# Kernel optimization log

Hardware: AMD Instinct MI355X
Metric: run time of the kernel (lower is better)

The kernel has to match this reference:

```python
import jax, jax.numpy as jnp
import numpy as np
import math

GROUPS = 32
EPS = 1e-5
NUM_HEADS = 8


def group_norm(x, gamma, beta):
    # x: [B, C, H, W]; normalize within each of GROUPS channel groups over (C/G, H, W)
    B, C, H, W = x.shape
    xg = x.reshape(B, GROUPS, C // GROUPS, H, W)
    mean = jnp.mean(xg, axis=(2, 3, 4), keepdims=True)
    var = jnp.var(xg, axis=(2, 3, 4), keepdims=True)
    xn = ((xg - mean) * jax.lax.rsqrt(var + EPS)).reshape(B, C, H, W)
    return xn * gamma[None, :, None, None] + beta[None, :, None, None]


def setup_inputs() -> dict:
    key = jax.random.key(0)
    ks = jax.random.split(key, 10)
    C = 512
    B, H, W = 2, 64, 64
    s = 1.0 / math.sqrt(C)
    return {
        "x": jax.random.normal(ks[0], (B, C, H, W), jnp.float32),
        "gamma": jnp.ones((C,), jnp.float32),
        "beta": jnp.zeros((C,), jnp.float32),
        "Wq": jax.random.normal(ks[1], (C, C), jnp.float32) * s,
        "bq": jax.random.normal(ks[2], (C,), jnp.float32) * 0.01,
        "Wk": jax.random.normal(ks[3], (C, C), jnp.float32) * s,
        "bk": jax.random.normal(ks[4], (C,), jnp.float32) * 0.01,
        "Wv": jax.random.normal(ks[5], (C, C), jnp.float32) * s,
        "bv": jax.random.normal(ks[6], (C,), jnp.float32) * 0.01,
        "Wo": jax.random.normal(ks[7], (C, C), jnp.float32) * s,
        "bo": jax.random.normal(ks[8], (C,), jnp.float32) * 0.01,
    }


def reference(x, gamma, beta, Wq, bq, Wk, bk, Wv, bv, Wo, bo):
    B, C, H, W = x.shape
    N = H * W
    hd = C // NUM_HEADS
    h = group_norm(x, gamma, beta)
    h = h.reshape(B, C, N).transpose(0, 2, 1)  # [B, N, C]
    # torch nn.Linear: y = x @ W.T + b
    q = (h @ Wq.T + bq).reshape(B, N, NUM_HEADS, hd)
    k = (h @ Wk.T + bk).reshape(B, N, NUM_HEADS, hd)
    v = (h @ Wv.T + bv).reshape(B, N, NUM_HEADS, hd)
    scale = 1.0 / math.sqrt(hd)
    attn = jnp.einsum('bihd,bjhd->bijh', q, k) * scale  # [B, N, N, heads]
    attn = jax.nn.softmax(attn, axis=2)
    o = jnp.einsum('bijh,bjhd->bihd', attn, v).reshape(B, N, C)
    o = o @ Wo.T + bo
    o = o.transpose(0, 2, 1).reshape(B, C, H, W)
    return x + o
```

## Files before the change

### kernel.cpp

```cpp
#include <hip/hip_runtime.h>
#include <cstdint>
#include <cstddef>

typedef __bf16 bf16x8 __attribute__((ext_vector_type(8)));
typedef float f32x4 __attribute__((ext_vector_type(4)));
typedef float f32x16 __attribute__((ext_vector_type(16)));
typedef unsigned short ushort8 __attribute__((ext_vector_type(8)));
typedef unsigned u32x2 __attribute__((ext_vector_type(2)));
typedef float f4 __attribute__((ext_vector_type(4)));

__device__ __forceinline__ unsigned short f2bf(float f) {
    __bf16 b = (__bf16)f;
    return *(unsigned short*)&b;
}
__device__ __forceinline__ unsigned pk2bf(float a, float b) {
    __bf16 x = (__bf16)a, y = (__bf16)b;
    unsigned short ux = *(unsigned short*)&x, uy = *(unsigned short*)&y;
    return (unsigned)ux | ((unsigned)uy << 16);
}
__device__ __forceinline__ float bf2f(unsigned short u) {
    union { unsigned u; float f; } v; v.u = ((unsigned)u) << 16; return v.f;
}

#if __has_builtin(__builtin_amdgcn_exp2f)
#define EXP2(x) __builtin_amdgcn_exp2f(x)
#else
#define EXP2(x) exp2f(x)
#endif

__device__ __forceinline__ void pl32swap(unsigned& x, unsigned& y) {
#if __has_builtin(__builtin_amdgcn_permlane32_swap)
    auto r = __builtin_amdgcn_permlane32_swap(x, y, false, false);
    x = r[0]; y = r[1];
#else
    unsigned xs = (unsigned)__shfl_xor((int)x, 32, 64);
    unsigned ys = (unsigned)__shfl_xor((int)y, 32, 64);
    bool lo = ((threadIdx.x & 63) < 32);
    unsigned nx = lo ? x : ys;
    unsigned ny = lo ? xs : y;
    x = nx; y = ny;
#endif
}

#define GLL(g, l) __builtin_amdgcn_global_load_lds( \
    (__attribute__((address_space(1))) void*)(g), \
    (__attribute__((address_space(3))) void*)(l), 16, 0, 0)

#define CS 0.18033688011112042f

__global__ __launch_bounds__(256) void convert_w(
    const float* __restrict__ wq, const float* __restrict__ wk,
    const float* __restrict__ wv, const float* __restrict__ wo,
    unsigned short* __restrict__ out)
{
    int i = blockIdx.x * 256 + threadIdx.x;
    const float* src = (i < 262144) ? wq : (i < 524288) ? wk : (i < 786432) ? wv : wo;
    out[i] = f2bf(src[i & 262143]);
}

__global__ __launch_bounds__(256) void gn_stats(
    const float* __restrict__ x, float* __restrict__ part)
{
    const int q = blockIdx.x, bg = blockIdx.y;
    const f4* xv = (const f4*)(x + (size_t)bg * 65536 + q * 16384);
    float s = 0.f, sq = 0.f;
    for (int i = threadIdx.x; i < 4096; i += 256) {
        f4 v = xv[i];
        s  += v.x + v.y + v.z + v.w;
        sq += v.x * v.x + v.y * v.y + v.z * v.z + v.w * v.w;
    }
    #pragma unroll
    for (int off = 32; off > 0; off >>= 1) {
        s  += __shfl_xor(s, off, 64);
        sq += __shfl_xor(sq, off, 64);
    }
    __shared__ float red[8];
    const int w = threadIdx.x >> 6, lane = threadIdx.x & 63;
    if (lane == 0) { red[w] = s; red[4 + w] = sq; }
    __syncthreads();
    if (threadIdx.x == 0) {
        part[(bg * 4 + q) * 2]     = red[0] + red[1] + red[2] + red[3];
        part[(bg * 4 + q) * 2 + 1] = red[4] + red[5] + red[6] + red[7];
    }
}

__global__ __launch_bounds__(256) void gn_apply(
    const float* __restrict__ x, const float* __restrict__ gamma,
    const float* __restrict__ beta, const float* __restrict__ part,
    unsigned short* __restrict__ h)
{
    const int q = blockIdx.x, bg = blockIdx.y;
    const int b = bg >> 5, g = bg & 31;
    float s = 0.f, sq = 0.f;
    #pragma unroll
    for (int j = 0; j < 4; ++j) {
        s  += part[(bg * 4 + j) * 2];
        sq += part[(bg * 4 + j) * 2 + 1];
    }
    const float mean = s * (1.f / 65536.f);
    const float rstd = rsqrtf(sq * (1.f / 65536.f) - mean * mean + 1e-5f);

    float gm[16], bt[16];
    #pragma unroll
    for (int c = 0; c < 16; ++c) {
        gm[c] = gamma[g * 16 + c] * rstd;
        bt[c] = beta[g * 16 + c];
    }
    const float* xg = x + (size_t)bg * 65536;
    const int n0 = q * 1024 + threadIdx.x * 4;
    float val[16][4];
    #pragma unroll
    for (int c = 0; c < 16; ++c) {
        f4 v = *(const f4*)&xg[(size_t)c * 4096 + n0];
        val[c][0] = (v.x - mean) * gm[c] + bt[c];
        val[c][1] = (v.y - mean) * gm[c] + bt[c];
        val[c][2] = (v.z - mean) * gm[c] + bt[c];
        val[c][3] = (v.w - mean) * gm[c] + bt[c];
    }
    #pragma unroll
    for (int nn = 0; nn < 4; ++nn) {
        ushort8 v0, v1;
        #pragma unroll
        for (int c = 0; c < 8; ++c)  v0[c]     = f2bf(val[c][nn]);
        #pragma unroll
        for (int c = 8; c < 16; ++c) v1[c - 8] = f2bf(val[c][nn]);
        unsigned short* dst = h + ((size_t)(b * 4096 + n0 + nn)) * 512 + g * 16;
        *(ushort8*)dst = v0;
        *(ushort8*)(dst + 8) = v1;
    }
}

template <int MODE>
__global__ __launch_bounds__(256, 2) void gemm_bt(
    const unsigned short* __restrict__ A,
    const unsigned short* __restrict__ Bt,
    const float* __restrict__ bias0,
    const float* __restrict__ bias1,
    const float* __restrict__ bias2,
    const float* __restrict__ resid,
    void* __restrict__ outp,
    unsigned short* __restrict__ vtout,
    int M, int N, int K)
{
    __shared__ __attribute__((aligned(16))) unsigned short As[128 * 32];
    __shared__ __attribute__((aligned(16))) unsigned short Bs[128 * 32];
    const int t = threadIdx.x;
    const int w = t >> 6, lane = t & 63;
    const int l15 = lane & 15, l4 = lane >> 4;
    const int bm = blockIdx.y, bn = blockIdx.x;
    const int wm = (w >> 1) * 64, wn = (w & 1) * 64;

    f32x4 acc[4][4] = {};

    const int srow = t >> 2;
    const int sc8  = (t & 3) * 8;

    const unsigned short* gA0 = A  + (size_t)(bm * 128 + srow) * K + sc8;
    const unsigned short* gA1 = gA0 + (size_t)64 * K;
    const unsigned short* gB0 = Bt + (size_t)(bn * 128 + srow) * K + sc8;
    const unsigned short* gB1 = gB0 + (size_t)64 * K;
    unsigned short* lA0 = &As[w * 512];
    unsigned short* lA1 = &As[2048 + w * 512];
    unsigned short* lB0 = &Bs[w * 512];
    unsigned short* lB1 = &Bs[2048 + w * 512];

    for (int k0 = 0; k0 < K; k0 += 32) {
        __syncthreads();
        GLL(gA0 + k0, lA0);
        GLL(gA1 + k0, lA1);
        GLL(gB0 + k0, lB0);
        GLL(gB1 + k0, lB1);
        __syncthreads();

        bf16x8 af[4], bfr[4];
        #pragma unroll
        for (int mt = 0; mt < 4; ++mt)
            af[mt] = *(const bf16x8*)&As[(wm + mt * 16 + l15) * 32 + l4 * 8];
        #pragma unroll
        for (int nt = 0; nt < 4; ++nt)
            bfr[nt] = *(const bf16x8*)&Bs[(wn + nt * 16 + l15) * 32 + l4 * 8];
        #pragma unroll
        for (int mt = 0; mt < 4; ++mt)
            #pragma unroll
            for (int nt = 0; nt < 4; ++nt)
                acc[mt][nt] = __builtin_amdgcn_mfma_f32_16x16x32_bf16(
                    af[mt], bfr[nt], acc[mt][nt], 0, 0, 0);
    }

    if (MODE == 0) {
        unsigned short* outB = (unsigned short*)outp;
        #pragma unroll
        for (int nt = 0; nt < 4; ++nt) {
            int col = bn * 128 + wn + nt * 16 + l15;
            const float* bp = (col < 512) ? bias0 : (col < 1024) ? bias1 : bias2;
            float bv = bp[col & 511];
            if (col < 1024) {
                float sc = (col < 512) ? CS : 1.0f;
                #pragma unroll
                for (int mt = 0; mt < 4; ++mt)
                    #pragma unroll
                    for (int r = 0; r < 4; ++r) {
                        int row = bm * 128 + wm + mt * 16 + l4 * 4 + r;
                        outB[(size_t)row * N + col] = f2bf((acc[mt][nt][r] + bv));
                        if (col < 512)
                            outB[(size_t)row * N + col] = f2bf((acc[mt][nt][r] + bv) * CS);
                    }
            } else {
                int hd = col - 1024;
                #pragma unroll
                for (int mt = 0; mt < 4; ++mt) {
                    int m = bm * 128 + wm + mt * 16 + l4 * 4;
                    int bb = m >> 12, n = m & 4095;
                    unsigned u0 = pk2bf(acc[mt][nt][0] + bv, acc[mt][nt][1] + bv);
                    unsigned u1 = pk2bf(acc[mt][nt][2] + bv, acc[mt][nt][3] + bv);
                    unsigned short* dst = vtout +
                        ((size_t)(bb * 8 + (hd >> 6)) * 64 + (hd & 63)) * 4096 + n;
                    *(u32x2*)dst = (u32x2){u0, u1};
                }
            }
        }
    } else {
        float* outF = (float*)outp;
        #pragma unroll
        for (int mt = 0; mt < 4; ++mt)
            #pragma unroll
            for (int nt = 0; nt < 4; ++nt)
                #pragma unroll
                for (int r = 0; r < 4; ++r) {
                    int c = bm * 128 + wm + mt * 16 + l4 * 4 + r;
                    int m = bn * 128 + wn + nt * 16 + l15;
                    int b = m >> 12, n = m & 4095;
                    size_t idx = ((size_t)(b * 512 + c)) * 4096 + n;
                    outF[idx] = acc[mt][nt][r] + bias0[c] + resid[idx];
                }
    }
}

__global__ __launch_bounds__(256, 2) void attn_kernel(
    const unsigned short* __restrict__ qkv, const unsigned short* __restrict__ vt,
    unsigned short* __restrict__ opart, float* __restrict__ lbuf)
{
    __shared__ __attribute__((aligned(16))) unsigned short Ks[64][72];
    __shared__ __attribute__((aligned(16))) unsigned short Vts[64][72];
    __shared__ __attribute__((aligned(16))) unsigned short Oepi[256][72];

    const int bh = blockIdx.y, b = bh >> 3, h = bh & 7;
    const int qbase = blockIdx.x * 256;
    const int s = blockIdx.z, ks0 = s * 2048;
    const int t = threadIdx.x, w = t >> 6, lane = t & 63;
    const int l31 = lane & 31, h5 = lane >> 5;

    const unsigned short* Qg = qkv + ((size_t)(b * 4096 + qbase + w * 64)) * 1536 + h * 64;
    const unsigned short* Kg = qkv + ((size_t)(b * 4096 + ks0)) * 1536 + 512 + h * 64;
    const unsigned short* Vg = vt + ((size_t)bh) * 64 * 4096 + ks0;

    bf16x8 qf[2][4];
    #pragma unroll
    for (int qt = 0; qt < 2; ++qt)
        #pragma unroll
        for (int kc = 0; kc < 4; ++kc)
            qf[qt][kc] = *(const bf16x8*)(Qg + (size_t)(qt * 32 + l31) * 1536 + kc * 16 + h5 * 8);

    f32x16 Oacc[2][2] = {};
    float li[2] = {0.f, 0.f};

    const int sr = t >> 2, sc = (t & 3) * 16;
    const unsigned short* gK = Kg + (size_t)sr * 1536 + sc;
    const unsigned short* gV = Vg + (size_t)sr * 4096 + sc;
    unsigned short* lK = &Ks[sr][sc];
    unsigned short* lV = &Vts[sr][sc];

    ushort8 kr[2], vr[2];
    kr[0] = *(const ushort8*)(gK);
    kr[1] = *(const ushort8*)(gK + 8);
    vr[0] = *(const ushort8*)(gV);
    vr[1] = *(const ushort8*)(gV + 8);

    for (int kt = 0; kt < 32; ++kt) {
        __syncthreads();
        *(ushort8*)(lK)     = kr[0];
        *(ushort8*)(lK + 8) = kr[1];
        *(ushort8*)(lV)     = vr[0];
        *(ushort8*)(lV + 8) = vr[1];
        __syncthreads();
        if (kt < 31) {
            const unsigned short* nk = gK + (size_t)(kt + 1) * 64 * 1536;
            const unsigned short* nv = gV + (kt + 1) * 64;
            kr[0] = *(const ushort8*)(nk);
            kr[1] = *(const ushort8*)(nk + 8);
            vr[0] = *(const ushort8*)(nv);
            vr[1] = *(const ushort8*)(nv + 8);
        }

        f32x16 St[2][2] = {};
        #pragma unroll
        for (int ct = 0; ct < 2; ++ct)
            #pragma unroll
            for (int kc = 0; kc < 4; ++kc) {
                bf16x8 kf = *(const bf16x8*)&Ks[ct * 32 + l31][kc * 16 + h5 * 8];
                St[0][ct] = __builtin_amdgcn_mfma_f32_32x32x16_bf16(kf, qf[0][kc], St[0][ct], 0, 0, 0);
                St[1][ct] = __builtin_amdgcn_mfma_f32_32x32x16_bf16(kf, qf[1][kc], St[1][ct], 0, 0, 0);
            }

        union PU { unsigned u[4]; bf16x8 v; };
        PU pf[2][4];
        #pragma unroll
        for (int qt = 0; qt < 2; ++qt) {
            #pragma unroll
            for (int ct = 0; ct < 2; ++ct)
                #pragma unroll
                for (int r = 0; r < 16; ++r)
                    St[qt][ct][r] = EXP2(St[qt][ct][r]);
            float s0 = 0.f, s1 = 0.f;
            #pragma unroll
            for (int ct = 0; ct < 2; ++ct) {
                s0 += ((St[qt][ct][0] + St[qt][ct][1]) + (St[qt][ct][2] + St[qt][ct][3]))
                    + ((St[qt][ct][4] + St[qt][ct][5]) + (St[qt][ct][6] + St[qt][ct][7]));
                s1 += ((St[qt][ct][8] + St[qt][ct][9]) + (St[qt][ct][10] + St[qt][ct][11]))
                    + ((St[qt][ct][12] + St[qt][ct][13]) + (St[qt][ct][14] + St[qt][ct][15]));
            }
            li[qt] += s0 + s1;

            #pragma unroll
            for (int ct = 0; ct < 2; ++ct) {
                unsigned pk0 = pk2bf(St[qt][ct][0],  St[qt][ct][1]);
                unsigned pk1 = pk2bf(St[qt][ct][2],  St[qt][ct][3]);
                unsigned pk2 = pk2bf(St[qt][ct][4],  St[qt][ct][5]);
                unsigned pk3 = pk2bf(St[qt][ct][6],  St[qt][ct][7]);
                unsigned pk4 = pk2bf(St[qt][ct][8],  St[qt][ct][9]);
                unsigned pk5 = pk2bf(St[qt][ct][10], St[qt][ct][11]);
                unsigned pk6 = pk2bf(St[qt][ct][12], St[qt][ct][13]);
                unsigned pk7 = pk2bf(St[qt][ct][14], St[qt][ct][15]);
                pl32swap(pk0, pk2); pl32swap(pk1, pk3);
                pl32swap(pk4, pk6); pl32swap(pk5, pk7);
                pf[qt][ct * 2].u[0] = pk0; pf[qt][ct * 2].u[1] = pk1;
                pf[qt][ct * 2].u[2] = pk2; pf[qt][ct * 2].u[3] = pk3;
                pf[qt][ct * 2 + 1].u[0] = pk4; pf[qt][ct * 2 + 1].u[1] = pk5;
                pf[qt][ct * 2 + 1].u[2] = pk6; pf[qt][ct * 2 + 1].u[3] = pk7;
            }
        }

        #pragma unroll
        for (int kk = 0; kk < 4; ++kk)
            #pragma unroll
            for (int dt = 0; dt < 2; ++dt) {
                bf16x8 vf = *(const bf16x8*)&Vts[dt * 32 + l31][kk * 16 + h5 * 8];
                Oacc[dt][0] = __builtin_amdgcn_mfma_f32_32x32x16_bf16(vf, pf[0][kk].v, Oacc[dt][0], 0, 0, 0);
                Oacc[dt][1] = __builtin_amdgcn_mfma_f32_32x32x16_bf16(vf, pf[1][kk].v, Oacc[dt][1], 0, 0, 0);
            }
    }

    #pragma unroll
    for (int qt = 0; qt < 2; ++qt) {
        float lf = li[qt] + __shfl_xor(li[qt], 32, 64);
        if (h5 == 0)
            lbuf[((size_t)s * 16 + bh) * 4096 + qbase + w * 64 + qt * 32 + l31] = lf;
        #pragma unroll
        for (int dt = 0; dt < 2; ++dt)
            #pragma unroll
            for (int p = 0; p < 8; ++p) {
                int d = dt * 32 + 2 * (p & 1) + 8 * (p >> 1) + 4 * h5;
                unsigned u = pk2bf(Oacc[dt][qt][2 * p], Oacc[dt][qt][2 * p + 1]);
                *(unsigned*)&Oepi[w * 64 + qt * 32 + l31][d] = u;
            }
    }
    unsigned short* Og = opart + (((size_t)s * 16 + bh) * 4096 + qbase + w * 64) * 64;
    #pragma unroll
    for (int c8 = 0; c8 < 8; ++c8) {
        ushort8 val = *(const ushort8*)&Oepi[w * 64 + lane][c8 * 8];
        *(ushort8*)(Og + (size_t)lane * 64 + c8 * 8) = val;
    }
}

__global__ __launch_bounds__(256) void combine_o(
    const unsigned short* __restrict__ opart, const float* __restrict__ lbuf,
    unsigned short* __restrict__ o)
{
    int gid = blockIdx.x * 256 + threadIdx.x;
    int row = gid >> 3, c8 = gid & 7;
    int bh = row >> 12, q = row & 4095;
    int b = bh >> 3, h = bh & 7;
    float inv = 1.f / (lbuf[row] + lbuf[65536 + row]);
    ushort8 o0 = *(const ushort8*)(opart + (size_t)row * 64 + c8 * 8);
    ushort8 o1 = *(const ushort8*)(opart + (size_t)65536 * 64 + (size_t)row * 64 + c8 * 8);
    ushort8 r;
    #pragma unroll
    for (int i = 0; i < 8; ++i)
        r[i] = f2bf((bf2f(o0[i]) + bf2f(o1[i])) * inv);
    *(ushort8*)(o + ((size_t)(b * 4096 + q)) * 512 + h * 64 + c8 * 8) = r;
}

extern "C" void kernel_launch(void* const* d_in, const int* in_sizes, int n_in,
                              void* d_out, int out_size, void* d_ws, size_t ws_size,
                              hipStream_t stream) {
    const float* x     = (const float*)d_in[0];
    const float* gamma = (const float*)d_in[1];
    const float* beta  = (const float*)d_in[2];
    const float* Wq    = (const float*)d_in[3];
    const float* bq    = (const float*)d_in[4];
    const float* Wk    = (const float*)d_in[5];
    const float* bk    = (const float*)d_in[6];
    const float* Wv    = (const float*)d_in[7];
    const float* bv    = (const float*)d_in[8];
    const float* Wo    = (const float*)d_in[9];
    const float* bo    = (const float*)d_in[10];
    float* out = (float*)d_out;

    char* ws = (char*)d_ws;
    const size_t MB = 1024 * 1024;
    unsigned short* h      = (unsigned short*)(ws);
    unsigned short* qkv    = (unsigned short*)(ws + 8 * MB);
    unsigned short* vtb    = (unsigned short*)(ws + 32 * MB);
    unsigned short* wb     = (unsigned short*)(ws + 40 * MB);
    float*          gnpart = (float*)(ws + 42 * MB);
    unsigned short* opart  = (unsigned short*)(ws + 43 * MB);
    float*          lbuf   = (float*)(ws + 59 * MB);

    convert_w<<<dim3(4096), dim3(256), 0, stream>>>(Wq, Wk, Wv, Wo, wb);
    gn_stats<<<dim3(4, 64), dim3(256), 0, stream>>>(x, gnpart);
    gn_apply<<<dim3(4, 64), dim3(256), 0, stream>>>(x, gamma, beta, gnpart, h);

    gemm_bt<0><<<dim3(12, 64), dim3(256), 0, stream>>>(
        h, wb, bq, bk, bv, nullptr, qkv, vtb, 8192, 1536, 512);

    attn_kernel<<<dim3(16, 16, 2), dim3(256), 0, stream>>>(qkv, vtb, opart, lbuf);
    combine_o<<<dim3(2048), dim3(256), 0, stream>>>(opart, lbuf, h);

    gemm_bt<1><<<dim3(64, 4), dim3(256), 0, stream>>>(
        wb + 786432, h, bo, nullptr, nullptr, x, out, nullptr, 512, 8192, 512);
}
```

Before: 221.4 us.

## Split attention keys four ways, separate Q/K buffers, shrink output GEMM tile

Attention now splits the key range into four chunks instead of two, and raises occupancy to 4 blocks per SM by dropping the LDS epilogue staging buffer and writing partial outputs directly. The combine kernel sums four partials. Q and K are written to separate contiguous 512-wide buffers, which removes the 1536 stride and the redundant double store for Q. The output-projection GEMM uses 64-row tiles to double its grid. Together these aim to increase parallelism and occupancy, at the cost of more partial-output traffic and uncoalesced direct stores.

Result: slower. 668.5 us (+202.0%).

```diff
diff --git a/kernel.cpp b/kernel.cpp
--- a/kernel.cpp
+++ b/kernel.cpp
@@ -130,7 +130,7 @@
     }
 }
 
-template <int MODE>
+template <int MODE, int BM>
 __global__ __launch_bounds__(256, 2) void gemm_bt(
     const unsigned short* __restrict__ A,
     const unsigned short* __restrict__ Bt,
@@ -139,48 +139,48 @@
     const float* __restrict__ bias2,
     const float* __restrict__ resid,
     void* __restrict__ outp,
+    unsigned short* __restrict__ kout,
     unsigned short* __restrict__ vtout,
     int M, int N, int K)
 {
-    __shared__ __attribute__((aligned(16))) unsigned short As[128 * 32];
+    constexpr int MT = BM / 32;
+    __shared__ __attribute__((aligned(16))) unsigned short As[BM * 32];
     __shared__ __attribute__((aligned(16))) unsigned short Bs[128 * 32];
     const int t = threadIdx.x;
     const int w = t >> 6, lane = t & 63;
     const int l15 = lane & 15, l4 = lane >> 4;
     const int bm = blockIdx.y, bn = blockIdx.x;
-    const int wm = (w >> 1) * 64, wn = (w & 1) * 64;
-
-    f32x4 acc[4][4] = {};
+    const int wm = (w >> 1) * (BM / 2), wn = (w & 1) * 64;
+
+    f32x4 acc[MT][4] = {};
 
     const int srow = t >> 2;
     const int sc8  = (t & 3) * 8;
 
-    const unsigned short* gA0 = A  + (size_t)(bm * 128 + srow) * K + sc8;
-    const unsigned short* gA1 = gA0 + (size_t)64 * K;
+    const unsigned short* gA0 = A  + (size_t)(bm * BM + srow) * K + sc8;
     const unsigned short* gB0 = Bt + (size_t)(bn * 128 + srow) * K + sc8;
     const unsigned short* gB1 = gB0 + (size_t)64 * K;
     unsigned short* lA0 = &As[w * 512];
-    unsigned short* lA1 = &As[2048 + w * 512];
     unsigned short* lB0 = &Bs[w * 512];
     unsigned short* lB1 = &Bs[2048 + w * 512];
 
     for (int k0 = 0; k0 < K; k0 += 32) {
         __syncthreads();
         GLL(gA0 + k0, lA0);
-        GLL(gA1 + k0, lA1);
+        if (BM == 128) GLL(gA0 + (size_t)64 * K + k0, &As[2048 + w * 512]);
         GLL(gB0 + k0, lB0);
         GLL(gB1 + k0, lB1);
         __syncthreads();
 
-        bf16x8 af[4], bfr[4];
-        #pragma unroll
-        for (int mt = 0; mt < 4; ++mt)
+        bf16x8 af[MT], bfr[4];
+        #pragma unroll
+        for (int mt = 0; mt < MT; ++mt)
             af[mt] = *(const bf16x8*)&As[(wm + mt * 16 + l15) * 32 + l4 * 8];
         #pragma unroll
         for (int nt = 0; nt < 4; ++nt)
             bfr[nt] = *(const bf16x8*)&Bs[(wn + nt * 16 + l15) * 32 + l4 * 8];
         #pragma unroll
-        for (int mt = 0; mt < 4; ++mt)
+        for (int mt = 0; mt < MT; ++mt)
             #pragma unroll
             for (int nt = 0; nt < 4; ++nt)
                 acc[mt][nt] = __builtin_amdgcn_mfma_f32_16x16x32_bf16(
@@ -188,28 +188,28 @@
     }
 
     if (MODE == 0) {
-        unsigned short* outB = (unsigned short*)outp;
+        unsigned short* qout = (unsigned short*)outp;
         #pragma unroll
         for (int nt = 0; nt < 4; ++nt) {
             int col = bn * 128 + wn + nt * 16 + l15;
             const float* bp = (col < 512) ? bias0 : (col < 1024) ? bias1 : bias2;
             float bv = bp[col & 511];
             if (col < 1024) {
+                unsigned short* dst = (col < 512) ? qout : kout;
+                int cc = col & 511;
                 float sc = (col < 512) ? CS : 1.0f;
                 #pragma unroll
-                for (int mt = 0; mt < 4; ++mt)
+                for (int mt = 0; mt < MT; ++mt)
                     #pragma unroll
                     for (int r = 0; r < 4; ++r) {
-                        int row = bm * 128 + wm + mt * 16 + l4 * 4 + r;
-                        outB[(size_t)row * N + col] = f2bf((acc[mt][nt][r] + bv));
-                        if (col < 512)
-                            outB[(size_t)row * N + col] = f2bf((acc[mt][nt][r] + bv) * CS);
+                        int row = bm * BM + wm + mt * 16 + l4 * 4 + r;
+                        dst[(size_t)row * 512 + cc] = f2bf((acc[mt][nt][r] + bv) * sc);
                     }
             } else {
                 int hd = col - 1024;
                 #pragma unroll
-                for (int mt = 0; mt < 4; ++mt) {
-                    int m = bm * 128 + wm + mt * 16 + l4 * 4;
+                for (int mt = 0; mt < MT; ++mt) {
+                    int m = bm * BM + wm + mt * 16 + l4 * 4;
                     int bb = m >> 12, n = m & 4095;
                     unsigned u0 = pk2bf(acc[mt][nt][0] + bv, acc[mt][nt][1] + bv);
                     unsigned u1 = pk2bf(acc[mt][nt][2] + bv, acc[mt][nt][3] + bv);
@@ -222,12 +222,12 @@
     } else {
         float* outF = (float*)outp;
         #pragma unroll
-        for (int mt = 0; mt < 4; ++mt)
+        for (int mt = 0; mt < MT; ++mt)
             #pragma unroll
             for (int nt = 0; nt < 4; ++nt)
                 #pragma unroll
                 for (int r = 0; r < 4; ++r) {
-                    int c = bm * 128 + wm + mt * 16 + l4 * 4 + r;
+                    int c = bm * BM + wm + mt * 16 + l4 * 4 + r;
                     int m = bn * 128 + wn + nt * 16 + l15;
                     int b = m >> 12, n = m & 4095;
                     size_t idx = ((size_t)(b * 512 + c)) * 4096 + n;
@@ -236,22 +236,22 @@
     }
 }
 
-__global__ __launch_bounds__(256, 2) void attn_kernel(
-    const unsigned short* __restrict__ qkv, const unsigned short* __restrict__ vt,
+__global__ __launch_bounds__(256, 4) void attn_kernel(
+    const unsigned short* __restrict__ qb, const unsigned short* __restrict__ kb,
+    const unsigned short* __restrict__ vt,
     unsigned short* __restrict__ opart, float* __restrict__ lbuf)
 {
     __shared__ __attribute__((aligned(16))) unsigned short Ks[64][72];
     __shared__ __attribute__((aligned(16))) unsigned short Vts[64][72];
-    __shared__ __attribute__((aligned(16))) unsigned short Oepi[256][72];
 
     const int bh = blockIdx.y, b = bh >> 3, h = bh & 7;
     const int qbase = blockIdx.x * 256;
-    const int s = blockIdx.z, ks0 = s * 2048;
+    const int s = blockIdx.z, ks0 = s * 1024;
     const int t = threadIdx.x, w = t >> 6, lane = t & 63;
     const int l31 = lane & 31, h5 = lane >> 5;
 
-    const unsigned short* Qg = qkv + ((size_t)(b * 4096 + qbase + w * 64)) * 1536 + h * 64;
-    const unsigned short* Kg = qkv + ((size_t)(b * 4096 + ks0)) * 1536 + 512 + h * 64;
+    const unsigned short* Qg = qb + ((size_t)(b * 4096 + qbase + w * 64)) * 512 + h * 64;
+    const unsigned short* Kg = kb + ((size_t)(b * 4096 + ks0)) * 512 + h * 64;
     const unsigned short* Vg = vt + ((size_t)bh) * 64 * 4096 + ks0;
 
     bf16x8 qf[2][4];
@@ -259,13 +259,13 @@
     for (int qt = 0; qt < 2; ++qt)
         #pragma unroll
         for (int kc = 0; kc < 4; ++kc)
-            qf[qt][kc] = *(const bf16x8*)(Qg + (size_t)(qt * 32 + l31) * 1536 + kc * 16 + h5 * 8);
+            qf[qt][kc] = *(const bf16x8*)(Qg + (size_t)(qt * 32 + l31) * 512 + kc * 16 + h5 * 8);
 
     f32x16 Oacc[2][2] = {};
     float li[2] = {0.f, 0.f};
 
     const int sr = t >> 2, sc = (t & 3) * 16;
-    const unsigned short* gK = Kg + (size_t)sr * 1536 + sc;
+    const unsigned short* gK = Kg + (size_t)sr * 512 + sc;
     const unsigned short* gV = Vg + (size_t)sr * 4096 + sc;
     unsigned short* lK = &Ks[sr][sc];
     unsigned short* lV = &Vts[sr][sc];
@@ -276,15 +276,15 @@
     vr[0] = *(const ushort8*)(gV);
     vr[1] = *(const ushort8*)(gV + 8);
 
-    for (int kt = 0; kt < 32; ++kt) {
+    for (int kt = 0; kt < 16; ++kt) {
         __syncthreads();
         *(ushort8*)(lK)     = kr[0];
         *(ushort8*)(lK + 8) = kr[1];
         *(ushort8*)(lV)     = vr[0];
         *(ushort8*)(lV + 8) = vr[1];
         __syncthreads();
-        if (kt < 31) {
-            const unsigned short* nk = gK + (size_t)(kt + 1) * 64 * 1536;
+        if (kt < 15) {
+            const unsigned short* nk = gK + (size_t)(kt + 1) * 64 * 512;
             const unsigned short* nv = gV + (kt + 1) * 64;
             kr[0] = *(const ushort8*)(nk);
             kr[1] = *(const ushort8*)(nk + 8);
@@ -353,22 +353,17 @@
     #pragma unroll
     for (int qt = 0; qt < 2; ++qt) {
         float lf = li[qt] + __shfl_xor(li[qt], 32, 64);
-        if (h5 == 0)
-            lbuf[((size_t)s * 16 + bh) * 4096 + qbase + w * 64 + qt * 32 + l31] = lf;
+        size_t qrow = ((size_t)s * 16 + bh) * 4096 + qbase + w * 64 + qt * 32 + l31;
+        if (h5 == 0) lbuf[qrow] = lf;
+        unsigned short* orow = opart + qrow * 64;
         #pragma unroll
         for (int dt = 0; dt < 2; ++dt)
             #pragma unroll
             for (int p = 0; p < 8; ++p) {
                 int d = dt * 32 + 2 * (p & 1) + 8 * (p >> 1) + 4 * h5;
                 unsigned u = pk2bf(Oacc[dt][qt][2 * p], Oacc[dt][qt][2 * p + 1]);
-                *(unsigned*)&Oepi[w * 64 + qt * 32 + l31][d] = u;
-            }
-    }
-    unsigned short* Og = opart + (((size_t)s * 16 + bh) * 4096 + qbase + w * 64) * 64;
-    #pragma unroll
-    for (int c8 = 0; c8 < 8; ++c8) {
-        ushort8 val = *(const ushort8*)&Oepi[w * 64 + lane][c8 * 8];
-        *(ushort8*)(Og + (size_t)lane * 64 + c8 * 8) = val;
+                *(unsigned*)(orow + d) = u;
+            }
     }
 }
 
@@ -380,13 +375,18 @@
     int row = gid >> 3, c8 = gid & 7;
     int bh = row >> 12, q = row & 4095;
     int b = bh >> 3, h = bh & 7;
-    float inv = 1.f / (lbuf[row] + lbuf[65536 + row]);
-    ushort8 o0 = *(const ushort8*)(opart + (size_t)row * 64 + c8 * 8);
-    ushort8 o1 = *(const ushort8*)(opart + (size_t)65536 * 64 + (size_t)row * 64 + c8 * 8);
+    float lsum = lbuf[row] + lbuf[65536 + row] + lbuf[131072 + row] + lbuf[196608 + row];
+    float inv = 1.f / lsum;
+    float acc[8] = {};
+    #pragma unroll
+    for (int sp = 0; sp < 4; ++sp) {
+        ushort8 ov = *(const ushort8*)(opart + ((size_t)sp * 65536 + row) * 64 + c8 * 8);
+        #pragma unroll
+        for (int i = 0; i < 8; ++i) acc[i] += bf2f(ov[i]);
+    }
     ushort8 r;
     #pragma unroll
-    for (int i = 0; i < 8; ++i)
-        r[i] = f2bf((bf2f(o0[i]) + bf2f(o1[i])) * inv);
+    for (int i = 0; i < 8; ++i) r[i] = f2bf(acc[i] * inv);
     *(ushort8*)(o + ((size_t)(b * 4096 + q)) * 512 + h * 64 + c8 * 8) = r;
 }
 
@@ -408,24 +408,26 @@
 
     char* ws = (char*)d_ws;
     const size_t MB = 1024 * 1024;
-    unsigned short* h      = (unsigned short*)(ws);
-    unsigned short* qkv    = (unsigned short*)(ws + 8 * MB);
-    unsigned short* vtb    = (unsigned short*)(ws + 32 * MB);
-    unsigned short* wb     = (unsigned short*)(ws + 40 * MB);
-    float*          gnpart = (float*)(ws + 42 * MB);
-    unsigned short* opart  = (unsigned short*)(ws + 43 * MB);
-    float*          lbuf   = (float*)(ws + 59 * MB);
+    unsigned short* qbuf   = (unsigned short*)(ws);
+    unsigned short* kbuf   = (unsigned short*)(ws + 8 * MB);
+    unsigned short* obuf   = kbuf;
+    unsigned short* vtb    = (unsigned short*)(ws + 16 * MB);
+    unsigned short* h      = (unsigned short*)(ws + 24 * MB);
+    unsigned short* opart  = (unsigned short*)(ws + 24 * MB);
+    unsigned short* wb     = (unsigned short*)(ws + 56 * MB);
+    float*          gnpart = (float*)(ws + 58 * MB);
+    float*          lbuf   = (float*)(ws + 58 * MB + 256 * 1024);
 
     convert_w<<<dim3(4096), dim3(256), 0, stream>>>(Wq, Wk, Wv, Wo, wb);
     gn_stats<<<dim3(4, 64), dim3(256), 0, stream>>>(x, gnpart);
     gn_apply<<<dim3(4, 64), dim3(256), 0, stream>>>(x, gamma, beta, gnpart, h);
 
-    gemm_bt<0><<<dim3(12, 64), dim3(256), 0, stream>>>(
-        h, wb, bq, bk, bv, nullptr, qkv, vtb, 8192, 1536, 512);
-
-    attn_kernel<<<dim3(16, 16, 2), dim3(256), 0, stream>>>(qkv, vtb, opart, lbuf);
-    combine_o<<<dim3(2048), dim3(256), 0, stream>>>(opart, lbuf, h);
-
-    gemm_bt<1><<<dim3(64, 4), dim3(256), 0, stream>>>(
-        wb + 786432, h, bo, nullptr, nullptr, x, out, nullptr, 512, 8192, 512);
-}
+    gemm_bt<0, 128><<<dim3(12, 64), dim3(256), 0, stream>>>(
+        h, wb, bq, bk, bv, nullptr, qbuf, kbuf, vtb, 8192, 1536, 512);
+
+    attn_kernel<<<dim3(16, 16, 4), dim3(256), 0, stream>>>(qbuf, kbuf, vtb, opart, lbuf);
+    combine_o<<<dim3(2048), dim3(256), 0, stream>>>(opart, lbuf, obuf);
+
+    gemm_bt<1, 64><<<dim3(64, 8), dim3(256), 0, stream>>>(
+        wb + 786432, obuf, bo, nullptr, nullptr, x, out, nullptr, nullptr, 512, 8192, 512);
+}
```
